# Performance work log

Measured on AMD Instinct MI355X. Metric: run time of the kernel, lower is better.

Reference implementation:

```python
import jax, jax.numpy as jnp
import numpy as np

B, N, C = 8, 4096, 256
HID = 256          # HGNN conv hidden width
MLP_HID = 64       # final_mlp_hidden_width


def setup_inputs() -> dict:
    key = jax.random.key(0)
    ks = jax.random.split(key, 10)
    s = lambda fan_in: 1.0 / np.sqrt(fan_in)
    states = jax.random.normal(ks[0], (B, N, C), dtype=jnp.float32)
    # symmetric-normalized hypergraph Laplacian-like propagation matrix [N, N]
    A = jax.random.uniform(ks[1], (N, N), dtype=jnp.float32)
    A = 0.5 * (A + A.T)
    d = jnp.sum(A, axis=1)
    G = A / jnp.sqrt(d[:, None] * d[None, :])
    W1 = jax.random.uniform(ks[2], (C, HID), jnp.float32, -s(C), s(C))
    b1 = jnp.zeros((HID,), jnp.float32)
    W2 = jax.random.uniform(ks[3], (HID, HID), jnp.float32, -s(HID), s(HID))
    b2 = jnp.zeros((HID,), jnp.float32)
    Wm1 = jax.random.uniform(ks[4], (HID, MLP_HID), jnp.float32, -s(HID), s(HID))
    bm1 = jnp.zeros((MLP_HID,), jnp.float32)
    Wm2 = jax.random.uniform(ks[5], (MLP_HID, 1), jnp.float32, -s(MLP_HID), s(MLP_HID))
    bm2 = jnp.zeros((1,), jnp.float32)
    return {"states": states, "G": G, "W1": W1, "b1": b1, "W2": W2,
            "b2": b2, "Wm1": Wm1, "bm1": bm1, "Wm2": Wm2, "bm2": bm2}


def reference(states, G, W1, b1, W2, b2, Wm1, bm1, Wm2, bm2):
    # HGNN conv 1: G @ (X W1 + b1), ReLU.  states: [B,N,C]
    h = jnp.einsum('nm,bmh->bnh', G, states @ W1 + b1)
    h = jax.nn.relu(h)
    # HGNN conv 2
    h = jnp.einsum('nm,bmh->bnh', G, h @ W2 + b2)
    h = jax.nn.relu(h)
    # final MLP: hidden -> 64 -> 1 (per-node scalar state value)
    h = jax.nn.relu(h @ Wm1 + bm1)
    return h @ Wm2 + bm2  # [B, N, 1]
```

## Files before the change

kernel.cpp:

```cpp
#include <hip/hip_runtime.h>

#define N_NODES 4096
#define C_IN    256
#define HID     256
#define BATCH   8
#define R_TOT   32768

typedef unsigned short u16;
typedef short s8v  __attribute__((ext_vector_type(8)));
typedef float f4v  __attribute__((ext_vector_type(4)));
typedef u16   u16x4 __attribute__((ext_vector_type(4)));

#define MFMA(a,b,c) __builtin_amdgcn_mfma_f32_16x16x32_bf16((a),(b),(c),0,0,0)

__device__ __forceinline__ u16 bf_rne(float x) {
    unsigned u = __float_as_uint(x);
    u += 0x7fffu + ((u >> 16) & 1u);
    return (u16)(u >> 16);
}
__device__ __forceinline__ float bf_f(u16 h) {
    return __uint_as_float(((unsigned)h) << 16);
}

__device__ __forceinline__ void glds16(const void* g, void* l) {
    __builtin_amdgcn_global_load_lds(
        (const __attribute__((address_space(1))) void*)g,
        (__attribute__((address_space(3))) void*)l, 16, 0, 0);
}


__global__ void splitGX_k(const float* __restrict__ G, u16* __restrict__ Gh,
                          const float* __restrict__ X, u16* __restrict__ Xh) {
    const int nG = 4194304;
    const int nTot = nG + 2097152;
    int i = blockIdx.x * blockDim.x + threadIdx.x;
    const int stride = gridDim.x * blockDim.x;
    for (; i < nTot; i += stride) {
        const float4* src; u16x4* dst; int j;
        if (i < nG) { src = (const float4*)G; dst = (u16x4*)Gh; j = i; }
        else        { src = (const float4*)X; dst = (u16x4*)Xh; j = i - nG; }
        float4 x = src[j];
        u16x4 hh;
        hh[0] = bf_rne(x.x); hh[1] = bf_rne(x.y);
        hh[2] = bf_rne(x.z); hh[3] = bf_rne(x.w);
        dst[j] = hh;
    }
}

__global__ void splitT2_k(const float* __restrict__ W1, u16* __restrict__ W1th,
                          const float* __restrict__ W2, u16* __restrict__ W2th) {
    const float* in = blockIdx.y ? W2 : W1;
    u16* oh = blockIdx.y ? W2th : W1th;
    const int c = blockIdx.x;
    const int h = threadIdx.x;
    oh[h * 256 + c] = bf_rne(in[c * 256 + h]);
}

__global__ __launch_bounds__(256, 2) void gemm_small_k(
    const u16* __restrict__ Ah, const u16* __restrict__ Bh,
    const float* __restrict__ bias, u16* __restrict__ Oh)
{
    __shared__ u16 sAh[4096], sBh[4096];
    const int tid = threadIdx.x;
    const int w = tid >> 6, lane = tid & 63;
    const int i0 = blockIdx.x * 128;
    const int r0 = blockIdx.y * 128;
    const int lr = lane & 15, lk = lane >> 4;
    const int wr = (w >> 1) * 64, wc = (w & 1) * 64;
    const int kslot = (lk ^ ((lr >> 1) & 3)) * 8;
    const int cb = ((lane & 3) ^ ((lane >> 3) & 3)) * 8;

    const u16 *pAh[2], *pBh[2];
#pragma unroll
    for (int j = 0; j < 2; ++j) {
        const int ra = i0 + (w * 2 + j) * 16 + (lane >> 2);
        pAh[j] = Ah + (size_t)ra * 256 + cb;
        const int rb = r0 + (w * 2 + j) * 16 + (lane >> 2);
        pBh[j] = Bh + (size_t)rb * 256 + cb;
    }

    f4v acc[4][4] = {};

    for (int kt = 0; kt < 8; ++kt) {
#pragma unroll
        for (int j = 0; j < 2; ++j) {
            glds16(pAh[j] + kt * 32, sAh + (w * 2 + j) * 512);
            glds16(pBh[j] + kt * 32, sBh + (w * 2 + j) * 512);
        }
        __syncthreads();

        s8v fah[4], fbh[4];
#pragma unroll
        for (int m = 0; m < 4; ++m) {
            fah[m] = *(const s8v*)(sAh + (wr + m * 16 + lr) * 32 + kslot);
            fbh[m] = *(const s8v*)(sBh + (wc + m * 16 + lr) * 32 + kslot);
        }
#pragma unroll
        for (int m = 0; m < 4; ++m)
#pragma unroll
            for (int n = 0; n < 4; ++n)
                acc[m][n] = MFMA(fah[m], fbh[n], acc[m][n]);
        __syncthreads();
    }

#pragma unroll
    for (int m = 0; m < 4; ++m) {
#pragma unroll
        for (int q = 0; q < 4; ++q) {
            const int rowg = i0 + wr + m * 16 + lk * 4 + q;
            const float bv = bias[rowg];
#pragma unroll
            for (int n = 0; n < 4; ++n) {
                const int colg = r0 + wc + n * 16 + lr;
                float v = acc[m][n][q] + bv;
                Oh[(size_t)rowg * R_TOT + colg] = bf_rne(v);
            }
        }
    }
}

__global__ __launch_bounds__(512, 2) void gemm_big_k(
    const u16* __restrict__ Gh, const u16* __restrict__ Th,
    u16* __restrict__ Hh)
{
    extern __shared__ u16 lds[];
    const int tid = threadIdx.x;
    const int w = tid >> 6, l = tid & 63;
    const int n0 = blockIdx.x * 256;
    const int h0 = blockIdx.y * 128;
    const int b  = blockIdx.z;
    const int lr = l & 15, lk = l >> 4;
    const int wm = w >> 1, wn = w & 1;
    const int sl0 = ((lk)     ^ (lr & 7)) * 8;
    const int sl1 = ((4 + lk) ^ (lr & 7)) * 8;

    const int srow  = l >> 3;
    const int sslot = ((l & 7) ^ srow) * 8;

    const u16* pA0 = Gh + (size_t)(n0 + 8 * w        + srow) * 4096 + sslot;
    const u16* pA1 = Gh + (size_t)(n0 + 8 * (w + 8)  + srow) * 4096 + sslot;
    const u16* pA2 = Gh + (size_t)(n0 + 8 * (w + 16) + srow) * 4096 + sslot;
    const u16* pA3 = Gh + (size_t)(n0 + 8 * (w + 24) + srow) * 4096 + sslot;
    const u16* pB0 = Th + (size_t)(h0 + 8 * w       + srow) * R_TOT + (size_t)b * 4096 + sslot;
    const u16* pB1 = Th + (size_t)(h0 + 8 * (w + 8) + srow) * R_TOT + (size_t)b * 4096 + sslot;

    const int dA0 = w * 512, dA1 = (w + 8) * 512, dA2 = (w + 16) * 512, dA3 = (w + 24) * 512;
    const int dB0 = 16384 + w * 512, dB1 = 16384 + (w + 8) * 512;

    f4v acc[4][4] = {};

#define STAGE6(STG) do {                                                       \
    u16* Ls = lds + (STG) * 24576;                                             \
    glds16(pA0, Ls + dA0); glds16(pA1, Ls + dA1);                              \
    glds16(pA2, Ls + dA2); glds16(pA3, Ls + dA3);                              \
    glds16(pB0, Ls + dB0); glds16(pB1, Ls + dB1);                              \
    pA0 += 64; pA1 += 64; pA2 += 64; pA3 += 64; pB0 += 64; pB1 += 64;          \
} while (0)

#define KTILE(CUR, STG, DO_STAGE, VMODE) do {                                  \
    const u16* Lc = lds + (CUR) * 24576;                                       \
    u16* Ls = lds + (STG) * 24576;                                             \
                                  \
    { s8v fa[4], fb[4];                                                        \
      _Pragma("unroll") for (int m = 0; m < 4; ++m)                            \
          fa[m] = *(const s8v*)(Lc + (wm * 64 + m * 16 + lr) * 64 + sl0);      \
      _Pragma("unroll") for (int n = 0; n < 4; ++n)                            \
          fb[n] = *(const s8v*)(Lc + 16384 + (wn * 64 + n * 16 + lr) * 64 + sl0); \
      if (DO_STAGE) { glds16(pA0, Ls + dA0); glds16(pA1, Ls + dA1);            \
                      glds16(pB0, Ls + dB0); }                                 \
      __builtin_amdgcn_s_barrier();                                            \
      __builtin_amdgcn_s_setprio(1);                                           \
      _Pragma("unroll") for (int m = 0; m < 4; ++m)                            \
          _Pragma("unroll") for (int n = 0; n < 4; ++n)                        \
              acc[m][n] = MFMA(fa[m], fb[n], acc[m][n]);                       \
      __builtin_amdgcn_s_setprio(0);                                           \
      __builtin_amdgcn_s_barrier(); }                                          \
                     \
    { s8v fa[4], fb[4];                                                        \
      _Pragma("unroll") for (int m = 0; m < 4; ++m)                            \
          fa[m] = *(const s8v*)(Lc + (wm * 64 + m * 16 + lr) * 64 + sl1);      \
      _Pragma("unroll") for (int n = 0; n < 4; ++n)                            \
          fb[n] = *(const s8v*)(Lc + 16384 + (wn * 64 + n * 16 + lr) * 64 + sl1); \
      if (DO_STAGE) { glds16(pA2, Ls + dA2); glds16(pA3, Ls + dA3);            \
                      glds16(pB1, Ls + dB1);                                   \
                      pA0 += 64; pA1 += 64; pA2 += 64; pA3 += 64;              \
                      pB0 += 64; pB1 += 64; }                                  \
      __builtin_amdgcn_s_barrier();                                            \
      __builtin_amdgcn_s_setprio(1);                                           \
      _Pragma("unroll") for (int m = 0; m < 4; ++m)                            \
          _Pragma("unroll") for (int n = 0; n < 4; ++n)                        \
              acc[m][n] = MFMA(fa[m], fb[n], acc[m][n]);                       \
      __builtin_amdgcn_s_setprio(0); }                                         \
    if (VMODE == 0)      asm volatile("s_waitcnt vmcnt(6)" ::: "memory");      \
    else if (VMODE == 1) asm volatile("s_waitcnt vmcnt(0)" ::: "memory");      \
    if (VMODE != 2) __builtin_amdgcn_s_barrier();                              \
    __builtin_amdgcn_sched_barrier(0);                                         \
} while (0)

    STAGE6(0);
    STAGE6(1);
    asm volatile("s_waitcnt vmcnt(6)" ::: "memory");
    __builtin_amdgcn_s_barrier();
    __builtin_amdgcn_sched_barrier(0);

    for (int it = 0; it < 20; ++it) {
        KTILE(0, 2, 1, 0);
        KTILE(1, 0, 1, 0);
        KTILE(2, 1, 1, 0);
    }
    KTILE(0, 2, 1, 0);
    KTILE(1, 0, 1, 0);
    KTILE(2, 1, 0, 1);
    KTILE(0, 2, 0, 2);

#undef STAGE6
#undef KTILE

    const size_t obase = ((size_t)b * 4096 + n0 + wm * 64 + lk * 4) * 256
                       + h0 + wn * 64 + lr;
#pragma unroll
    for (int m = 0; m < 4; ++m)
#pragma unroll
        for (int n = 0; n < 4; ++n)
#pragma unroll
            for (int q = 0; q < 4; ++q) {
                float v = acc[m][n][q];
                v = v > 0.f ? v : 0.f;
                Hh[obase + (size_t)(m * 16 + q) * 256 + n * 16] = bf_rne(v);
            }
}

__global__ __launch_bounds__(256) void mlp_k(
    const u16* __restrict__ Hh, const float* __restrict__ Wm1,
    const float* __restrict__ bm1, const float* __restrict__ Wm2,
    const float* __restrict__ bm2, float* __restrict__ out)
{
    __shared__ u16 sB[16384];
    const int tid = threadIdx.x;
    const int w = tid >> 6, l = tid & 63;
    const int lr = l & 15, lk = l >> 4;

    for (int idx = tid; idx < 16384; idx += 256) {
        const int col = idx & 63, k = idx >> 6;
        const int slot = (k >> 3) ^ (col & 7);
        sB[col * 256 + slot * 8 + (k & 7)] = bf_rne(Wm1[k * 64 + col]);
    }
    __syncthreads();

    float bm1v[4], w2v[4];
#pragma unroll
    for (int n = 0; n < 4; ++n) {
        bm1v[n] = bm1[n * 16 + lr];
        w2v[n]  = Wm2[n * 16 + lr];
    }
    const float b2v = bm2[0];

    const int rowbase = blockIdx.x * 128 + w * 32;
    f4v acc[2][4] = {};
#pragma unroll
    for (int ks = 0; ks < 8; ++ks) {
        s8v fa[2], fb[4];
#pragma unroll
        for (int m = 0; m < 2; ++m)
            fa[m] = *(const s8v*)(Hh + (size_t)(rowbase + m * 16 + lr) * 256 + ks * 32 + lk * 8);
        const int slot = ((ks * 4 + lk) ^ (lr & 7)) * 8;
#pragma unroll
        for (int n = 0; n < 4; ++n)
            fb[n] = *(const s8v*)(sB + (n * 16 + lr) * 256 + slot);
#pragma unroll
        for (int m = 0; m < 2; ++m)
#pragma unroll
            for (int n = 0; n < 4; ++n)
                acc[m][n] = MFMA(fa[m], fb[n], acc[m][n]);
    }

#pragma unroll
    for (int m = 0; m < 2; ++m)
#pragma unroll
        for (int q = 0; q < 4; ++q) {
            float p = 0.f;
#pragma unroll
            for (int n = 0; n < 4; ++n) {
                float v = acc[m][n][q] + bm1v[n];
                v = v > 0.f ? v : 0.f;
                p += v * w2v[n];
            }
#pragma unroll
            for (int mask = 1; mask < 16; mask <<= 1)
                p += __shfl_xor(p, mask);
            if (lr == 0)
                out[rowbase + m * 16 + lk * 4 + q] = p + b2v;
        }
}

extern "C" void kernel_launch(void* const* d_in, const int* in_sizes, int n_in,
                              void* d_out, int out_size, void* d_ws, size_t ws_size,
                              hipStream_t stream) {
    (void)in_sizes; (void)n_in; (void)out_size; (void)ws_size;
    const float* X   = (const float*)d_in[0];
    const float* G   = (const float*)d_in[1];
    const float* W1  = (const float*)d_in[2];
    const float* b1  = (const float*)d_in[3];
    const float* W2  = (const float*)d_in[4];
    const float* b2  = (const float*)d_in[5];
    const float* Wm1 = (const float*)d_in[6];
    const float* bm1 = (const float*)d_in[7];
    const float* Wm2 = (const float*)d_in[8];
    const float* bm2 = (const float*)d_in[9];
    float* out = (float*)d_out;

    char* ws = (char*)d_ws;
    u16* Gh   = (u16*)(ws);
    u16* W1th = (u16*)(ws + 67108864u);
    u16* W2th = (u16*)(ws + 67371008u);
    u16* Tth  = (u16*)(ws + 67633152u);
    u16* XHh  = (u16*)(ws + 101187584u);

    splitGX_k<<<3072, 256, 0, stream>>>(G, Gh, X, XHh);
    splitT2_k<<<dim3(256, 2), 256, 0, stream>>>(W1, W1th, W2, W2th);

    gemm_small_k<<<dim3(2, 256), 256, 0, stream>>>(W1th, XHh, b1, Tth);
    gemm_big_k<<<dim3(16, 2, 8), 512, 147456, stream>>>(Gh, Tth, XHh);
    gemm_small_k<<<dim3(2, 256), 256, 0, stream>>>(W2th, XHh, b2, Tth);
    gemm_big_k<<<dim3(16, 2, 8), 512, 147456, stream>>>(Gh, Tth, XHh);
    mlp_k<<<256, 256, 0, stream>>>(XHh, Wm1, bm1, Wm2, bm2, out);
}
```

Baseline: 182.6 us.

## Fuse X bf16 conversion into first small GEMM and split big-GEMM k-tile into quarters

The separate fp32-to-bf16 conversion of the states tensor is removed from the split kernel. The first small GEMM now reads fp32 X directly, converting it while staging into LDS, which avoids writing and re-reading the bf16 copy. The big GEMM's per-k-tile body is split into four smaller phases of 8 MFMAs each, with the global-to-LDS loads interleaved. This is meant to overlap loads with compute more finely and to reduce live fragment registers, at the cost of more barriers per tile.

Result: no change. 181.2 us (-0.8%).

```diff
diff --git a/kernel.cpp b/kernel.cpp
--- a/kernel.cpp
+++ b/kernel.cpp
@@ -29,21 +29,16 @@
 }
 
 
-__global__ void splitGX_k(const float* __restrict__ G, u16* __restrict__ Gh,
-                          const float* __restrict__ X, u16* __restrict__ Xh) {
-    const int nG = 4194304;
-    const int nTot = nG + 2097152;
+__global__ void splitG_k(const float* __restrict__ G, u16* __restrict__ Gh) {
+    const int n4 = 4194304;
     int i = blockIdx.x * blockDim.x + threadIdx.x;
     const int stride = gridDim.x * blockDim.x;
-    for (; i < nTot; i += stride) {
-        const float4* src; u16x4* dst; int j;
-        if (i < nG) { src = (const float4*)G; dst = (u16x4*)Gh; j = i; }
-        else        { src = (const float4*)X; dst = (u16x4*)Xh; j = i - nG; }
-        float4 x = src[j];
+    for (; i < n4; i += stride) {
+        float4 x = ((const float4*)G)[i];
         u16x4 hh;
         hh[0] = bf_rne(x.x); hh[1] = bf_rne(x.y);
         hh[2] = bf_rne(x.z); hh[3] = bf_rne(x.w);
-        dst[j] = hh;
+        ((u16x4*)Gh)[i] = hh;
     }
 }
 
@@ -56,7 +51,78 @@
     oh[h * 256 + c] = bf_rne(in[c * 256 + h]);
 }
 
-__global__ __launch_bounds__(256, 2) void gemm_small_k(
+__global__ __launch_bounds__(256, 2) void gemm_small1_k(
+    const u16* __restrict__ Ah, const float* __restrict__ Bf,
+    const float* __restrict__ bias, u16* __restrict__ Oh)
+{
+    __shared__ u16 sAh[4096], sBh[4096];
+    const int tid = threadIdx.x;
+    const int w = tid >> 6, lane = tid & 63;
+    const int i0 = blockIdx.x * 128;
+    const int r0 = blockIdx.y * 128;
+    const int lr = lane & 15, lk = lane >> 4;
+    const int wr = (w >> 1) * 64, wc = (w & 1) * 64;
+    const int kslot = (lk ^ ((lr >> 1) & 3)) * 8;
+    const int cb = ((lane & 3) ^ ((lane >> 3) & 3)) * 8;
+
+    const u16 *pAh[2];
+#pragma unroll
+    for (int j = 0; j < 2; ++j) {
+        const int ra = i0 + (w * 2 + j) * 16 + (lane >> 2);
+        pAh[j] = Ah + (size_t)ra * 256 + cb;
+    }
+
+    f4v acc[4][4] = {};
+
+    for (int kt = 0; kt < 8; ++kt) {
+#pragma unroll
+        for (int j = 0; j < 2; ++j)
+            glds16(pAh[j] + kt * 32, sAh + (w * 2 + j) * 512);
+#pragma unroll
+        for (int i = 0; i < 4; ++i) {
+            const int cc  = tid + i * 256;
+            const int row = cc >> 3;
+            const int col = (((((cc & 7) >> 1) ^ ((cc >> 4) & 3)) << 3)) | ((cc & 1) * 4);
+            const float* src = Bf + (size_t)(r0 + row) * 256 + kt * 32 + (cc & 7) * 4;
+            float4 x = *(const float4*)src;
+            u16x4 hh;
+            hh[0] = bf_rne(x.x); hh[1] = bf_rne(x.y);
+            hh[2] = bf_rne(x.z); hh[3] = bf_rne(x.w);
+            *(u16x4*)(sBh + row * 32 + col) = hh;
+        }
+        __syncthreads();
+
+        s8v fah[4], fbh[4];
+#pragma unroll
+        for (int m = 0; m < 4; ++m) {
+            fah[m] = *(const s8v*)(sAh + (wr + m * 16 + lr) * 32 + kslot);
+            fbh[m] = *(const s8v*)(sBh + (wc + m * 16 + lr) * 32 + kslot);
+        }
+#pragma unroll
+        for (int m = 0; m < 4; ++m)
+#pragma unroll
+            for (int n = 0; n < 4; ++n)
+                acc[m][n] = MFMA(fah[m], fbh[n], acc[m][n]);
+        __syncthreads();
+    }
+
+#pragma unroll
+    for (int m = 0; m < 4; ++m) {
+#pragma unroll
+        for (int q = 0; q < 4; ++q) {
+            const int rowg = i0 + wr + m * 16 + lk * 4 + q;
+            const float bv = bias[rowg];
+#pragma unroll
+            for (int n = 0; n < 4; ++n) {
+                const int colg = r0 + wc + n * 16 + lr;
+                float v = acc[m][n][q] + bv;
+                Oh[(size_t)rowg * R_TOT + colg] = bf_rne(v);
+            }
+        }
+    }
+}
+
+__global__ __launch_bounds__(256, 2) void gemm_small2_k(
     const u16* __restrict__ Ah, const u16* __restrict__ Bh,
     const float* __restrict__ bias, u16* __restrict__ Oh)
 {
@@ -157,50 +223,65 @@
     pA0 += 64; pA1 += 64; pA2 += 64; pA3 += 64; pB0 += 64; pB1 += 64;          \
 } while (0)
 
+#define BAR()  __builtin_amdgcn_s_barrier()
+#define PRIO1() __builtin_amdgcn_s_setprio(1)
+#define PRIO0() __builtin_amdgcn_s_setprio(0)
+
 #define KTILE(CUR, STG, DO_STAGE, VMODE) do {                                  \
     const u16* Lc = lds + (CUR) * 24576;                                       \
     u16* Ls = lds + (STG) * 24576;                                             \
+    s8v fa0[2], fa1[2], fb0[4], fb1[4];                                        \
                                   \
-    { s8v fa[4], fb[4];                                                        \
-      _Pragma("unroll") for (int m = 0; m < 4; ++m)                            \
-          fa[m] = *(const s8v*)(Lc + (wm * 64 + m * 16 + lr) * 64 + sl0);      \
-      _Pragma("unroll") for (int n = 0; n < 4; ++n)                            \
-          fb[n] = *(const s8v*)(Lc + 16384 + (wn * 64 + n * 16 + lr) * 64 + sl0); \
-      if (DO_STAGE) { glds16(pA0, Ls + dA0); glds16(pA1, Ls + dA1);            \
-                      glds16(pB0, Ls + dB0); }                                 \
-      __builtin_amdgcn_s_barrier();                                            \
-      __builtin_amdgcn_s_setprio(1);                                           \
-      _Pragma("unroll") for (int m = 0; m < 4; ++m)                            \
-          _Pragma("unroll") for (int n = 0; n < 4; ++n)                        \
-              acc[m][n] = MFMA(fa[m], fb[n], acc[m][n]);                       \
-      __builtin_amdgcn_s_setprio(0);                                           \
-      __builtin_amdgcn_s_barrier(); }                                          \
-                     \
-    { s8v fa[4], fb[4];                                                        \
-      _Pragma("unroll") for (int m = 0; m < 4; ++m)                            \
-          fa[m] = *(const s8v*)(Lc + (wm * 64 + m * 16 + lr) * 64 + sl1);      \
-      _Pragma("unroll") for (int n = 0; n < 4; ++n)                            \
-          fb[n] = *(const s8v*)(Lc + 16384 + (wn * 64 + n * 16 + lr) * 64 + sl1); \
-      if (DO_STAGE) { glds16(pA2, Ls + dA2); glds16(pA3, Ls + dA3);            \
-                      glds16(pB1, Ls + dB1);                                   \
-                      pA0 += 64; pA1 += 64; pA2 += 64; pA3 += 64;              \
-                      pB0 += 64; pB1 += 64; }                                  \
-      __builtin_amdgcn_s_barrier();                                            \
-      __builtin_amdgcn_s_setprio(1);                                           \
-      _Pragma("unroll") for (int m = 0; m < 4; ++m)                            \
-          _Pragma("unroll") for (int n = 0; n < 4; ++n)                        \
-              acc[m][n] = MFMA(fa[m], fb[n], acc[m][n]);                       \
-      __builtin_amdgcn_s_setprio(0); }                                         \
+    _Pragma("unroll") for (int m = 0; m < 2; ++m)                              \
+        fa0[m] = *(const s8v*)(Lc + (wm * 64 + m * 16 + lr) * 64 + sl0);       \
+    _Pragma("unroll") for (int n = 0; n < 4; ++n)                              \
+        fb0[n] = *(const s8v*)(Lc + 16384 + (wn * 64 + n * 16 + lr) * 64 + sl0); \
+    if (DO_STAGE) { glds16(pA0, Ls + dA0); glds16(pA1, Ls + dA1); }            \
+    BAR(); PRIO1();                                                            \
+    _Pragma("unroll") for (int m = 0; m < 2; ++m)                              \
+        _Pragma("unroll") for (int n = 0; n < 4; ++n)                          \
+            acc[m][n] = MFMA(fa0[m], fb0[n], acc[m][n]);                       \
+    PRIO0(); BAR();                                                            \
+                                      \
+    _Pragma("unroll") for (int m = 0; m < 2; ++m)                              \
+        fa1[m] = *(const s8v*)(Lc + (wm * 64 + (m + 2) * 16 + lr) * 64 + sl0); \
+    if (DO_STAGE) { glds16(pA2, Ls + dA2); glds16(pA3, Ls + dA3); }            \
+    BAR(); PRIO1();                                                            \
+    _Pragma("unroll") for (int m = 0; m < 2; ++m)                              \
+        _Pragma("unroll") for (int n = 0; n < 4; ++n)                          \
+            acc[m + 2][n] = MFMA(fa1[m], fb0[n], acc[m + 2][n]);               \
+    PRIO0(); BAR();                                                            \
+                                     \
+    _Pragma("unroll") for (int m = 0; m < 2; ++m)                              \
+        fa0[m] = *(const s8v*)(Lc + (wm * 64 + m * 16 + lr) * 64 + sl1);       \
+    _Pragma("unroll") for (int n = 0; n < 4; ++n)                              \
+        fb1[n] = *(const s8v*)(Lc + 16384 + (wn * 64 + n * 16 + lr) * 64 + sl1); \
+    if (DO_STAGE) { glds16(pB0, Ls + dB0); }                                   \
+    BAR(); PRIO1();                                                            \
+    _Pragma("unroll") for (int m = 0; m < 2; ++m)                              \
+        _Pragma("unroll") for (int n = 0; n < 4; ++n)                          \
+            acc[m][n] = MFMA(fa0[m], fb1[n], acc[m][n]);                       \
+    PRIO0(); BAR();                                                            \
+                           \
+    _Pragma("unroll") for (int m = 0; m < 2; ++m)                              \
+        fa1[m] = *(const s8v*)(Lc + (wm * 64 + (m + 2) * 16 + lr) * 64 + sl1); \
+    if (DO_STAGE) { glds16(pB1, Ls + dB1);                                     \
+        pA0 += 64; pA1 += 64; pA2 += 64; pA3 += 64; pB0 += 64; pB1 += 64; }    \
+    BAR(); PRIO1();                                                            \
+    _Pragma("unroll") for (int m = 0; m < 2; ++m)                              \
+        _Pragma("unroll") for (int n = 0; n < 4; ++n)                          \
+            acc[m + 2][n] = MFMA(fa1[m], fb1[n], acc[m + 2][n]);               \
+    PRIO0();                                                                   \
     if (VMODE == 0)      asm volatile("s_waitcnt vmcnt(6)" ::: "memory");      \
     else if (VMODE == 1) asm volatile("s_waitcnt vmcnt(0)" ::: "memory");      \
-    if (VMODE != 2) __builtin_amdgcn_s_barrier();                              \
+    if (VMODE != 2) BAR();                                                     \
     __builtin_amdgcn_sched_barrier(0);                                         \
 } while (0)
 
     STAGE6(0);
     STAGE6(1);
     asm volatile("s_waitcnt vmcnt(6)" ::: "memory");
-    __builtin_amdgcn_s_barrier();
+    BAR();
     __builtin_amdgcn_sched_barrier(0);
 
     for (int it = 0; it < 20; ++it) {
@@ -215,6 +296,9 @@
 
 #undef STAGE6
 #undef KTILE
+#undef BAR
+#undef PRIO1
+#undef PRIO0
 
     const size_t obase = ((size_t)b * 4096 + n0 + wm * 64 + lk * 4) * 256
                        + h0 + wn * 64 + lr;
@@ -314,14 +398,14 @@
     u16* W1th = (u16*)(ws + 67108864u);
     u16* W2th = (u16*)(ws + 67371008u);
     u16* Tth  = (u16*)(ws + 67633152u);
-    u16* XHh  = (u16*)(ws + 101187584u);
-
-    splitGX_k<<<3072, 256, 0, stream>>>(G, Gh, X, XHh);
+    u16* Hh   = (u16*)(ws + 101187584u);
+
+    splitG_k<<<2048, 256, 0, stream>>>(G, Gh);
     splitT2_k<<<dim3(256, 2), 256, 0, stream>>>(W1, W1th, W2, W2th);
 
-    gemm_small_k<<<dim3(2, 256), 256, 0, stream>>>(W1th, XHh, b1, Tth);
-    gemm_big_k<<<dim3(16, 2, 8), 512, 147456, stream>>>(Gh, Tth, XHh);
-    gemm_small_k<<<dim3(2, 256), 256, 0, stream>>>(W2th, XHh, b2, Tth);
-    gemm_big_k<<<dim3(16, 2, 8), 512, 147456, stream>>>(Gh, Tth, XHh);
-    mlp_k<<<256, 256, 0, stream>>>(XHh, Wm1, bm1, Wm2, bm2, out);
-}
+    gemm_small1_k<<<dim3(2, 256), 256, 0, stream>>>(W1th, X, b1, Tth);
+    gemm_big_k<<<dim3(16, 2, 8), 512, 147456, stream>>>(Gh, Tth, Hh);
+    gemm_small2_k<<<dim3(2, 256), 256, 0, stream>>>(W2th, Hh, b2, Tth);
+    gemm_big_k<<<dim3(16, 2, 8), 512, 147456, stream>>>(Gh, Tth, Hh);
+    mlp_k<<<256, 256, 0, stream>>>(Hh, Wm1, bm1, Wm2, bm2, out);
+}
```
